# Kernel tuning notes

Measured on AMD Instinct MI355X. Metric: run time of the kernel, lower is better.

The kernel has to match this reference:

```python
import jax, jax.numpy as jnp
import numpy as np

B, S, D, H = 2, 2048, 1024, 16
DH = D // H  # 64, matches Attention's hardcoded d_k=64 scale


def setup_inputs() -> dict:
    key = jax.random.key(0)
    kq, kk, kv, kw, kb = jax.random.split(key, 5)
    return {
        "q": jax.random.normal(kq, (B, S, D), dtype=jnp.float32),
        "k": jax.random.normal(kk, (B, S, D), dtype=jnp.float32),
        "v": jax.random.normal(kv, (B, S, D), dtype=jnp.float32),
        "w_o_w": jax.random.normal(kw, (D, D), dtype=jnp.float32) * 0.02,
        "w_o_b": jax.random.normal(kb, (D,), dtype=jnp.float32) * 0.02,
    }


def _to_heads(x):
    # [B,S,D] -> [B,H,S,DH]
    b, s, d = x.shape
    return x.reshape(b, s, H, DH).transpose(0, 2, 1, 3)


def reference(q, k, v, w_o_w, w_o_b):
    # pre-activation (F.relu) on raw q,k,v
    qh = _to_heads(jax.nn.relu(q))
    kh = _to_heads(jax.nn.relu(k))
    vh = _to_heads(jax.nn.relu(v))
    scale = 1.0 / jnp.sqrt(jnp.asarray(DH, dtype=q.dtype))
    # naive attention: full [B,H,S,S] score matrix, softmax over keys
    scores = jnp.einsum("bhsd,bhtd->bhst", qh, kh) * scale
    probs = jax.nn.softmax(scores, axis=-1)
    attn = jnp.einsum("bhst,bhtd->bhsd", probs, vh)
    # merge heads: [B,H,S,DH] -> [B,S,D]
    out = attn.transpose(0, 2, 1, 3).reshape(B, S, D)
    # output projection (nn.Linear applies x @ W.T + b) then post-activation
    out = out @ w_o_w.T + w_o_b
    return jax.nn.relu(out)
```

## Files before the change

### kernel.cpp

```cpp
#include <hip/hip_runtime.h>
#include <hip/hip_bf16.h>

#define Bc 2
#define Hc 16
#define Sc 2048
#define Dc 1024

typedef __attribute__((ext_vector_type(8))) short s16x8;
typedef __attribute__((ext_vector_type(4))) float f32x4;
typedef __attribute__((ext_vector_type(16))) float f32x16;

#define AS1 __attribute__((address_space(1)))
#define AS3 __attribute__((address_space(3)))

static __device__ __forceinline__ float fexp2(float x) {
#if __has_builtin(__builtin_amdgcn_exp2f)
    return __builtin_amdgcn_exp2f(x);
#else
    float r; asm("v_exp_f32 %0, %1" : "=v"(r) : "v"(x)); return r;
#endif
}

static __device__ __forceinline__ unsigned cvtpk(float lo, float hi) {
    unsigned r; asm("v_cvt_pk_bf16_f32 %0, %1, %2" : "=v"(r) : "v"(lo), "v"(hi));
    return r;
}

static __device__ __forceinline__ void plswap(unsigned &x, unsigned &y) {
#if __has_builtin(__builtin_amdgcn_permlane32_swap)
    typedef __attribute__((ext_vector_type(2))) unsigned int u32x2;
    u32x2 t = __builtin_amdgcn_permlane32_swap(x, y, false, false);
    x = t.x; y = t.y;
#else
    asm volatile("v_permlane32_swap_b32 %0, %1" : "+v"(x), "+v"(y));
#endif
}

static __device__ __forceinline__ unsigned short f2bf(float f) {
    union { float f; unsigned u; } x; x.f = f;
    unsigned r = x.u + 0x7fffu + ((x.u >> 16) & 1u);
    return (unsigned short)(r >> 16);
}

__global__ __launch_bounds__(256) void relu_cvt_heads(const float* __restrict__ src,
                                                      unsigned short* __restrict__ dst,
                                                      float scale) {
    long i = ((long)blockIdx.x * blockDim.x + threadIdx.x) * 4;
    if (i >= (long)Bc * Sc * Dc) return;
    int dh = (int)(i & 63);
    int h  = (int)((i >> 6) & (Hc - 1));
    int s  = (int)((i >> 10) & (Sc - 1));
    int b  = (int)(i >> 21);
    float4 v = *reinterpret_cast<const float4*>(src + i);
    long o = (((long)b * Hc + h) * Sc + s) * 64 + dh;
    ushort4 w;
    w.x = f2bf(fmaxf(v.x, 0.f) * scale);
    w.y = f2bf(fmaxf(v.y, 0.f) * scale);
    w.z = f2bf(fmaxf(v.z, 0.f) * scale);
    w.w = f2bf(fmaxf(v.w, 0.f) * scale);
    *reinterpret_cast<ushort4*>(dst + o) = w;
}

__global__ __launch_bounds__(256) void relu_cvt_vT(const float* __restrict__ v,
                                                   unsigned short* __restrict__ vt) {
    __shared__ unsigned short lds[64][66];
    const int tid = threadIdx.x;
    const int st = blockIdx.x & (Sc / 64 - 1);
    const int bh = blockIdx.x >> 5;
    const int b = bh >> 4, h = bh & 15;
#pragma unroll
    for (int i = 0; i < 4; ++i) {
        int srow = (tid >> 4) + i * 16;
        int scol = (tid & 15) * 4;
        float4 x = *(const float4*)(v + ((long)b * Sc + st * 64 + srow) * Dc + h * 64 + scol);
        lds[srow][scol + 0] = f2bf(fmaxf(x.x, 0.f));
        lds[srow][scol + 1] = f2bf(fmaxf(x.y, 0.f));
        lds[srow][scol + 2] = f2bf(fmaxf(x.z, 0.f));
        lds[srow][scol + 3] = f2bf(fmaxf(x.w, 0.f));
    }
    __syncthreads();
#pragma unroll
    for (int i = 0; i < 2; ++i) {
        int dh = (tid >> 3) + i * 32;
        int sc = (tid & 7) * 8;
        union { unsigned short u[8]; s16x8 v8; } o;
#pragma unroll
        for (int j = 0; j < 8; ++j) o.u[j] = lds[sc + j][dh];
        *(s16x8*)(vt + ((long)bh * 64 + dh) * Sc + st * 64 + sc) = o.v8;
    }
}

__global__ __launch_bounds__(256) void cvt_w(const float* __restrict__ src,
                                             unsigned short* __restrict__ dst) {
    long i = ((long)blockIdx.x * blockDim.x + threadIdx.x) * 4;
    if (i >= (long)Dc * Dc) return;
    float4 v = *reinterpret_cast<const float4*>(src + i);
    ushort4 w;
    w.x = f2bf(v.x); w.y = f2bf(v.y); w.z = f2bf(v.z); w.w = f2bf(v.w);
    *reinterpret_cast<ushort4*>(dst + i) = w;
}

__global__ __launch_bounds__(256, 2) void attn_lds(const unsigned short* __restrict__ qh,
                                                   const unsigned short* __restrict__ kh,
                                                   const unsigned short* __restrict__ vt,
                                                   unsigned short* __restrict__ xout) {
    __shared__ unsigned short Klds[2][64 * 64];
    __shared__ unsigned short Vlds[2][64 * 64];

    const int tid = threadIdx.x;
    const int l = tid & 63, w = tid >> 6;
    const int r32 = l & 31, hl = l >> 5;
    const int job = (blockIdx.x & 7) * 64 + (blockIdx.x >> 3);
    const int qb = job & 15;
    const int bh = job >> 4;

    const unsigned short* Qp = qh + ((long)bh * Sc + qb * 128 + w * 32) * 64;
    const unsigned short* Kp = kh + (long)bh * Sc * 64;
    const unsigned short* Vp = vt + (long)bh * 64 * Sc;

    s16x8 qbf[4];
#pragma unroll
    for (int ds = 0; ds < 4; ++ds)
        qbf[ds] = *(const s16x8*)(Qp + r32 * 64 + ds * 16 + hl * 8);

    f32x16 acc0 = {0,0,0,0,0,0,0,0,0,0,0,0,0,0,0,0};
    f32x16 acc1 = {0,0,0,0,0,0,0,0,0,0,0,0,0,0,0,0};
    float denom = 0.f;

    auto stage = [&](int buf, int kv0) {
#pragma unroll
        for (int j = 0; j < 2; ++j) {
            const int cbase = w * 64 + j * 256;
            const int chunk = cbase + l;
            const int row = chunk >> 3, cc = chunk & 7;
            const int scc = cc ^ (row & 7);
            const unsigned short* ksrc = Kp + (long)(kv0 + row) * 64 + scc * 8;
            const unsigned short* vsrc = Vp + (long)row * Sc + kv0 + scc * 8;
            __builtin_amdgcn_global_load_lds((const AS1 unsigned int*)(const void*)ksrc,
                                             (AS3 unsigned int*)(void*)&Klds[buf][cbase * 8],
                                             16, 0, 0);
            __builtin_amdgcn_global_load_lds((const AS1 unsigned int*)(const void*)vsrc,
                                             (AS3 unsigned int*)(void*)&Vlds[buf][cbase * 8],
                                             16, 0, 0);
        }
    };

    auto compute = [&](int buf) {
        const unsigned short* KB = &Klds[buf][0];
        const unsigned short* VB = &Vlds[buf][0];
        unsigned Bw[4][4];
#pragma unroll
        for (int kt = 0; kt < 2; ++kt) {
            f32x16 st = {0,0,0,0,0,0,0,0,0,0,0,0,0,0,0,0};
#pragma unroll
            for (int ds = 0; ds < 4; ++ds) {
                const int row = kt * 32 + r32;
                const int cc = ((ds * 2 + hl) ^ (row & 7));
                s16x8 ka = *(const s16x8*)(KB + row * 64 + cc * 8);
                st = __builtin_amdgcn_mfma_f32_32x32x16_bf16(ka, qbf[ds], st, 0, 0, 0);
            }
            float p[16];
#pragma unroll
            for (int i = 0; i < 16; ++i) p[i] = fexp2(st[i]);
            denom += (((p[0] + p[1]) + (p[2] + p[3])) + ((p[4] + p[5]) + (p[6] + p[7])))
                   + (((p[8] + p[9]) + (p[10] + p[11])) + ((p[12] + p[13]) + (p[14] + p[15])));
            unsigned a0 = cvtpk(p[0], p[1]),   b0 = cvtpk(p[2], p[3]);
            unsigned c0 = cvtpk(p[4], p[5]),   d0 = cvtpk(p[6], p[7]);
            unsigned a1 = cvtpk(p[8], p[9]),   b1 = cvtpk(p[10], p[11]);
            unsigned c1 = cvtpk(p[12], p[13]), d1 = cvtpk(p[14], p[15]);
            plswap(a0, c0); plswap(b0, d0);
            plswap(a1, c1); plswap(b1, d1);
            Bw[kt * 2 + 0][0] = a0; Bw[kt * 2 + 0][1] = b0;
            Bw[kt * 2 + 0][2] = c0; Bw[kt * 2 + 0][3] = d0;
            Bw[kt * 2 + 1][0] = a1; Bw[kt * 2 + 1][1] = b1;
            Bw[kt * 2 + 1][2] = c1; Bw[kt * 2 + 1][3] = d1;
        }
#pragma unroll
        for (int dt = 0; dt < 2; ++dt) {
#pragma unroll
            for (int s = 0; s < 4; ++s) {
                const int row = dt * 32 + r32;
                const int cc = ((s * 2 + hl) ^ (row & 7));
                s16x8 va = *(const s16x8*)(VB + row * 64 + cc * 8);
                union { unsigned u[4]; s16x8 v8; } bp;
                bp.u[0] = Bw[s][0]; bp.u[1] = Bw[s][1];
                bp.u[2] = Bw[s][2]; bp.u[3] = Bw[s][3];
                if (dt == 0)
                    acc0 = __builtin_amdgcn_mfma_f32_32x32x16_bf16(va, bp.v8, acc0, 0, 0, 0);
                else
                    acc1 = __builtin_amdgcn_mfma_f32_32x32x16_bf16(va, bp.v8, acc1, 0, 0, 0);
            }
        }
    };

    stage(0, 0);
    __syncthreads();
    int cur = 0;
    for (int t = 0; t < Sc / 64 - 1; ++t) {
        stage(cur ^ 1, (t + 1) * 64);
        compute(cur);
        __syncthreads();
        cur ^= 1;
    }
    compute(cur);

    float dn = denom + __shfl_xor(denom, 32);
    const float inv = 1.0f / dn;
    const int b = bh >> 4, h = bh & 15;
    unsigned short* Xrow = xout + ((long)b * Sc + qb * 128 + w * 32 + r32) * Dc + h * 64;
#pragma unroll
    for (int dt = 0; dt < 2; ++dt) {
        const f32x16& A = dt ? acc1 : acc0;
#pragma unroll
        for (int rg = 0; rg < 4; ++rg) {
            unsigned wlo = cvtpk(A[rg * 4 + 0] * inv, A[rg * 4 + 1] * inv);
            unsigned whi = cvtpk(A[rg * 4 + 2] * inv, A[rg * 4 + 3] * inv);
            uint2 wv; wv.x = wlo; wv.y = whi;
            *reinterpret_cast<uint2*>(Xrow + dt * 32 + rg * 8 + hl * 4) = wv;
        }
    }
}

__global__ __launch_bounds__(256, 2) void proj128(const unsigned short* __restrict__ X,
                                                  const unsigned short* __restrict__ Wb,
                                                  const float* __restrict__ bias,
                                                  float* __restrict__ out) {
    __shared__ unsigned short Xlds[2][128 * 64];
    __shared__ unsigned short Wlds[2][64 * 64];

    const int tid = threadIdx.x;
    const int l = tid & 63, w = tid >> 6;
    const int r32 = l & 31, hl = l >> 5;
    const int job = (blockIdx.x & 7) * 64 + (blockIdx.x >> 3);
    const int nb = job & 15;
    const int mb = job >> 4;

    const unsigned short* Xp = X + (long)mb * 128 * Dc;
    const unsigned short* Wp = Wb + (long)nb * 64 * Dc;

    f32x16 acc0 = {0,0,0,0,0,0,0,0,0,0,0,0,0,0,0,0};
    f32x16 acc1 = {0,0,0,0,0,0,0,0,0,0,0,0,0,0,0,0};

    auto stage = [&](int buf, int k0) {
#pragma unroll
        for (int j = 0; j < 4; ++j) {
            const int cbase = w * 256 + j * 64;
            const int chunk = cbase + l;
            const int row = chunk >> 3, cc = chunk & 7;
            const int scc = cc ^ (row & 7);
            const unsigned short* xsrc = Xp + (long)row * Dc + k0 + scc * 8;
            __builtin_amdgcn_global_load_lds((const AS1 unsigned int*)(const void*)xsrc,
                                             (AS3 unsigned int*)(void*)&Xlds[buf][cbase * 8],
                                             16, 0, 0);
        }
#pragma unroll
        for (int j = 0; j < 2; ++j) {
            const int cbase = w * 128 + j * 64;
            const int chunk = cbase + l;
            const int row = chunk >> 3, cc = chunk & 7;
            const int scc = cc ^ (row & 7);
            const unsigned short* wsrc = Wp + (long)row * Dc + k0 + scc * 8;
            __builtin_amdgcn_global_load_lds((const AS1 unsigned int*)(const void*)wsrc,
                                             (AS3 unsigned int*)(void*)&Wlds[buf][cbase * 8],
                                             16, 0, 0);
        }
    };

    auto compute = [&](int buf) {
        const unsigned short* XB = &Xlds[buf][0];
        const unsigned short* WB = &Wlds[buf][0];
#pragma unroll
        for (int ks = 0; ks < 4; ++ks) {
            const int arow = w * 32 + r32;
            const int acc_ = ((ks * 2 + hl) ^ (arow & 7));
            s16x8 af = *(const s16x8*)(XB + arow * 64 + acc_ * 8);
#pragma unroll
            for (int nt = 0; nt < 2; ++nt) {
                const int brow = nt * 32 + r32;
                const int bcc = ((ks * 2 + hl) ^ (brow & 7));
                s16x8 bf = *(const s16x8*)(WB + brow * 64 + bcc * 8);
                if (nt == 0)
                    acc0 = __builtin_amdgcn_mfma_f32_32x32x16_bf16(af, bf, acc0, 0, 0, 0);
                else
                    acc1 = __builtin_amdgcn_mfma_f32_32x32x16_bf16(af, bf, acc1, 0, 0, 0);
            }
        }
    };

    stage(0, 0);
    __syncthreads();
    int cur = 0;
    for (int t = 0; t < Dc / 64 - 1; ++t) {
        stage(cur ^ 1, (t + 1) * 64);
        compute(cur);
        __syncthreads();
        cur ^= 1;
    }
    compute(cur);

#pragma unroll
    for (int nt = 0; nt < 2; ++nt) {
        const f32x16& A = nt ? acc1 : acc0;
        const float bv = bias[nb * 64 + nt * 32 + r32];
#pragma unroll
        for (int j = 0; j < 16; ++j) {
            const int m = (j & 3) + 8 * (j >> 2) + 4 * hl;
            out[((long)(mb * 128 + w * 32 + m)) * Dc + nb * 64 + nt * 32 + r32] =
                fmaxf(A[j] + bv, 0.f);
        }
    }
}

extern "C" void kernel_launch(void* const* d_in, const int* in_sizes, int n_in,
                              void* d_out, int out_size, void* d_ws, size_t ws_size,
                              hipStream_t stream) {
    const float* q    = (const float*)d_in[0];
    const float* k    = (const float*)d_in[1];
    const float* v    = (const float*)d_in[2];
    const float* w    = (const float*)d_in[3];
    const float* bias = (const float*)d_in[4];
    float* out = (float*)d_out;

    unsigned short* ws = (unsigned short*)d_ws;
    unsigned short* qh = ws;
    unsigned short* kh = qh + 4194304;
    unsigned short* vt = kh + 4194304;
    unsigned short* wb = vt + 4194304;
    unsigned short* X  = wb + 1048576;

    const float QSCALE = 0.125f * 1.44269504088896340736f;
    relu_cvt_heads<<<4096, 256, 0, stream>>>(q, qh, QSCALE);
    relu_cvt_heads<<<4096, 256, 0, stream>>>(k, kh, 1.0f);
    relu_cvt_vT<<<1024, 256, 0, stream>>>(v, vt);
    cvt_w<<<1024, 256, 0, stream>>>(w, wb);
    attn_lds<<<Bc * Hc * (Sc / 128), 256, 0, stream>>>(qh, kh, vt, X);
    proj128<<<(Bc * Sc / 128) * (Dc / 64), 256, 0, stream>>>(X, wb, bias, out);
}
```

Baseline: 83.21 us.

## Restructure attention into single-wave blocks with barrier-free double-buffered LDS pipeline

Replaces the 4-wave, 128-query attention block with a one-wave kernel that handles 32 queries. Each wave stages its own 32-key K and V tiles into double-buffered LDS, using a swizzle adapted to the new V tile shape. Synchronisation moves from __syncthreads to an explicit vmcnt wait, and s_setprio is raised around the MFMA sections. This removes cross-wave barrier stalls and lets more independent waves hide latency, but K/V tiles are no longer shared across four waves, which raises L2/global traffic and issues one wasted wrapped-around prefetch on the final iteration.

```diff
diff --git a/kernel.cpp b/kernel.cpp
--- a/kernel.cpp
+++ b/kernel.cpp
@@ -12,6 +12,8 @@
 
 #define AS1 __attribute__((address_space(1)))
 #define AS3 __attribute__((address_space(3)))
+
+#define WAITVMC(N) asm volatile("s_waitcnt vmcnt(" #N ")" ::: "memory")
 
 static __device__ __forceinline__ float fexp2(float x) {
 #if __has_builtin(__builtin_amdgcn_exp2f)
@@ -100,21 +102,20 @@
     *reinterpret_cast<ushort4*>(dst + i) = w;
 }
 
-__global__ __launch_bounds__(256, 2) void attn_lds(const unsigned short* __restrict__ qh,
-                                                   const unsigned short* __restrict__ kh,
-                                                   const unsigned short* __restrict__ vt,
-                                                   unsigned short* __restrict__ xout) {
-    __shared__ unsigned short Klds[2][64 * 64];
-    __shared__ unsigned short Vlds[2][64 * 64];
-
-    const int tid = threadIdx.x;
-    const int l = tid & 63, w = tid >> 6;
+__global__ __launch_bounds__(64) void attn_pvt(const unsigned short* __restrict__ qh,
+                                               const unsigned short* __restrict__ kh,
+                                               const unsigned short* __restrict__ vt,
+                                               unsigned short* __restrict__ xout) {
+    __shared__ unsigned short Klds[2][32 * 64];
+    __shared__ unsigned short Vlds[2][64 * 32];
+
+    const int l = threadIdx.x;
     const int r32 = l & 31, hl = l >> 5;
-    const int job = (blockIdx.x & 7) * 64 + (blockIdx.x >> 3);
-    const int qb = job & 15;
-    const int bh = job >> 4;
-
-    const unsigned short* Qp = qh + ((long)bh * Sc + qb * 128 + w * 32) * 64;
+    const int job = (blockIdx.x & 7) * 256 + (blockIdx.x >> 3);
+    const int qt = job & (Sc / 32 - 1);
+    const int bh = job >> 6;
+
+    const unsigned short* Qp = qh + ((long)bh * Sc + qt * 32) * 64;
     const unsigned short* Kp = kh + (long)bh * Sc * 64;
     const unsigned short* Vp = vt + (long)bh * 64 * Sc;
 
@@ -129,18 +130,23 @@
 
     auto stage = [&](int buf, int kv0) {
 #pragma unroll
-        for (int j = 0; j < 2; ++j) {
-            const int cbase = w * 64 + j * 256;
-            const int chunk = cbase + l;
+        for (int j = 0; j < 4; ++j) {
+            const int chunk = j * 64 + l;
             const int row = chunk >> 3, cc = chunk & 7;
             const int scc = cc ^ (row & 7);
             const unsigned short* ksrc = Kp + (long)(kv0 + row) * 64 + scc * 8;
+            __builtin_amdgcn_global_load_lds((const AS1 unsigned int*)(const void*)ksrc,
+                                             (AS3 unsigned int*)(void*)&Klds[buf][chunk * 8],
+                                             16, 0, 0);
+        }
+#pragma unroll
+        for (int j = 0; j < 4; ++j) {
+            const int chunk = j * 64 + l;
+            const int row = chunk >> 2, cc = chunk & 3;
+            const int scc = cc ^ ((row >> 1) & 3);
             const unsigned short* vsrc = Vp + (long)row * Sc + kv0 + scc * 8;
-            __builtin_amdgcn_global_load_lds((const AS1 unsigned int*)(const void*)ksrc,
-                                             (AS3 unsigned int*)(void*)&Klds[buf][cbase * 8],
-                                             16, 0, 0);
             __builtin_amdgcn_global_load_lds((const AS1 unsigned int*)(const void*)vsrc,
-                                             (AS3 unsigned int*)(void*)&Vlds[buf][cbase * 8],
+                                             (AS3 unsigned int*)(void*)&Vlds[buf][chunk * 8],
                                              16, 0, 0);
         }
     };
@@ -148,66 +154,60 @@
     auto compute = [&](int buf) {
         const unsigned short* KB = &Klds[buf][0];
         const unsigned short* VB = &Vlds[buf][0];
-        unsigned Bw[4][4];
-#pragma unroll
-        for (int kt = 0; kt < 2; ++kt) {
-            f32x16 st = {0,0,0,0,0,0,0,0,0,0,0,0,0,0,0,0};
-#pragma unroll
-            for (int ds = 0; ds < 4; ++ds) {
-                const int row = kt * 32 + r32;
-                const int cc = ((ds * 2 + hl) ^ (row & 7));
-                s16x8 ka = *(const s16x8*)(KB + row * 64 + cc * 8);
-                st = __builtin_amdgcn_mfma_f32_32x32x16_bf16(ka, qbf[ds], st, 0, 0, 0);
-            }
-            float p[16];
-#pragma unroll
-            for (int i = 0; i < 16; ++i) p[i] = fexp2(st[i]);
-            denom += (((p[0] + p[1]) + (p[2] + p[3])) + ((p[4] + p[5]) + (p[6] + p[7])))
-                   + (((p[8] + p[9]) + (p[10] + p[11])) + ((p[12] + p[13]) + (p[14] + p[15])));
-            unsigned a0 = cvtpk(p[0], p[1]),   b0 = cvtpk(p[2], p[3]);
-            unsigned c0 = cvtpk(p[4], p[5]),   d0 = cvtpk(p[6], p[7]);
-            unsigned a1 = cvtpk(p[8], p[9]),   b1 = cvtpk(p[10], p[11]);
-            unsigned c1 = cvtpk(p[12], p[13]), d1 = cvtpk(p[14], p[15]);
-            plswap(a0, c0); plswap(b0, d0);
-            plswap(a1, c1); plswap(b1, d1);
-            Bw[kt * 2 + 0][0] = a0; Bw[kt * 2 + 0][1] = b0;
-            Bw[kt * 2 + 0][2] = c0; Bw[kt * 2 + 0][3] = d0;
-            Bw[kt * 2 + 1][0] = a1; Bw[kt * 2 + 1][1] = b1;
-            Bw[kt * 2 + 1][2] = c1; Bw[kt * 2 + 1][3] = d1;
-        }
-#pragma unroll
-        for (int dt = 0; dt < 2; ++dt) {
-#pragma unroll
-            for (int s = 0; s < 4; ++s) {
+        f32x16 st = {0,0,0,0,0,0,0,0,0,0,0,0,0,0,0,0};
+        __builtin_amdgcn_s_setprio(1);
+#pragma unroll
+        for (int ds = 0; ds < 4; ++ds) {
+            const int cc = ((ds * 2 + hl) ^ (r32 & 7));
+            s16x8 ka = *(const s16x8*)(KB + r32 * 64 + cc * 8);
+            st = __builtin_amdgcn_mfma_f32_32x32x16_bf16(ka, qbf[ds], st, 0, 0, 0);
+        }
+        __builtin_amdgcn_s_setprio(0);
+        float p[16];
+#pragma unroll
+        for (int i = 0; i < 16; ++i) p[i] = fexp2(st[i]);
+        denom += (((p[0] + p[1]) + (p[2] + p[3])) + ((p[4] + p[5]) + (p[6] + p[7])))
+               + (((p[8] + p[9]) + (p[10] + p[11])) + ((p[12] + p[13]) + (p[14] + p[15])));
+        unsigned a0 = cvtpk(p[0], p[1]),   b0 = cvtpk(p[2], p[3]);
+        unsigned c0 = cvtpk(p[4], p[5]),   d0 = cvtpk(p[6], p[7]);
+        unsigned a1 = cvtpk(p[8], p[9]),   b1 = cvtpk(p[10], p[11]);
+        unsigned c1 = cvtpk(p[12], p[13]), d1 = cvtpk(p[14], p[15]);
+        plswap(a0, c0); plswap(b0, d0);
+        plswap(a1, c1); plswap(b1, d1);
+        unsigned Bw[2][4] = {{a0, b0, c0, d0}, {a1, b1, c1, d1}};
+        __builtin_amdgcn_s_setprio(1);
+#pragma unroll
+        for (int ks = 0; ks < 2; ++ks) {
+            union { unsigned u[4]; s16x8 v8; } bp;
+            bp.u[0] = Bw[ks][0]; bp.u[1] = Bw[ks][1];
+            bp.u[2] = Bw[ks][2]; bp.u[3] = Bw[ks][3];
+#pragma unroll
+            for (int dt = 0; dt < 2; ++dt) {
                 const int row = dt * 32 + r32;
-                const int cc = ((s * 2 + hl) ^ (row & 7));
-                s16x8 va = *(const s16x8*)(VB + row * 64 + cc * 8);
-                union { unsigned u[4]; s16x8 v8; } bp;
-                bp.u[0] = Bw[s][0]; bp.u[1] = Bw[s][1];
-                bp.u[2] = Bw[s][2]; bp.u[3] = Bw[s][3];
+                const int cc = ((ks * 2 + hl) ^ ((row >> 1) & 3));
+                s16x8 va = *(const s16x8*)(VB + row * 32 + cc * 8);
                 if (dt == 0)
                     acc0 = __builtin_amdgcn_mfma_f32_32x32x16_bf16(va, bp.v8, acc0, 0, 0, 0);
                 else
                     acc1 = __builtin_amdgcn_mfma_f32_32x32x16_bf16(va, bp.v8, acc1, 0, 0, 0);
             }
         }
+        __builtin_amdgcn_s_setprio(0);
     };
 
     stage(0, 0);
-    __syncthreads();
-    int cur = 0;
-    for (int t = 0; t < Sc / 64 - 1; ++t) {
-        stage(cur ^ 1, (t + 1) * 64);
-        compute(cur);
-        __syncthreads();
-        cur ^= 1;
-    }
-    compute(cur);
+    for (int t = 0; t < Sc / 32; ++t) {
+        const int nxt = (t + 1) & (Sc / 32 - 1);
+        stage((t + 1) & 1, nxt * 32);
+        WAITVMC(8);
+        __builtin_amdgcn_sched_barrier(0);
+        compute(t & 1);
+    }
 
     float dn = denom + __shfl_xor(denom, 32);
     const float inv = 1.0f / dn;
     const int b = bh >> 4, h = bh & 15;
-    unsigned short* Xrow = xout + ((long)b * Sc + qb * 128 + w * 32 + r32) * Dc + h * 64;
+    unsigned short* Xrow = xout + ((long)b * Sc + qt * 32 + r32) * Dc + h * 64;
 #pragma unroll
     for (int dt = 0; dt < 2; ++dt) {
         const f32x16& A = dt ? acc1 : acc0;
@@ -333,6 +333,6 @@
     relu_cvt_heads<<<4096, 256, 0, stream>>>(k, kh, 1.0f);
     relu_cvt_vT<<<1024, 256, 0, stream>>>(v, vt);
     cvt_w<<<1024, 256, 0, stream>>>(w, wb);
-    attn_lds<<<Bc * Hc * (Sc / 128), 256, 0, stream>>>(qh, kh, vt, X);
+    attn_pvt<<<Bc * Hc * (Sc / 32), 64, 0, stream>>>(qh, kh, vt, X);
     proj128<<<(Bc * Sc / 128) * (Dc / 64), 256, 0, stream>>>(X, wb, bias, out);
 }
```

New measurement: 116.2 us. 1.4x slower.
